# Optimization experiments

Measured on AMD Instinct MI355X. Metric: run time of the kernel, lower is better.

Reference implementation:

```python
import jax, jax.numpy as jnp
import numpy as np

N = 50000   # n_nodes
E = 800000  # n_edges (directed)
D = 64      # feature dim (in = hidden = out = 64 per source)


def setup_inputs() -> dict:
    key = jax.random.key(0)
    ks = jax.random.split(key, 16)
    s = 0.1  # init scale
    inp = {
        "x": jax.random.normal(ks[0], (N, D), jnp.float32),
        "edge_index": jax.random.randint(ks[1], (2, E), 0, N),
        # GCNConv 1
        "W1": jax.random.normal(ks[2], (D, 64), jnp.float32) * s,
        "b1": jnp.zeros((64,), jnp.float32),
        # TransformerConv (heads=1): query/key/value + root (skip) linear
        "Wq": jax.random.normal(ks[3], (64, 64), jnp.float32) * s,
        "bq": jnp.zeros((64,), jnp.float32),
        "Wk": jax.random.normal(ks[4], (64, 64), jnp.float32) * s,
        "bk": jnp.zeros((64,), jnp.float32),
        "Wv": jax.random.normal(ks[5], (64, 64), jnp.float32) * s,
        "bv": jnp.zeros((64,), jnp.float32),
        "Ws": jax.random.normal(ks[6], (64, 64), jnp.float32) * s,
        "bs": jnp.zeros((64,), jnp.float32),
        # GCNConv 2
        "W2": jax.random.normal(ks[7], (64, D), jnp.float32) * s,
        "b2": jnp.zeros((D,), jnp.float32),
    }
    return inp


def gcn_conv(x, W, b, src, dst, n):
    """PyG GCNConv: symmetric normalization with self-loops, then scatter-add."""
    xw = x @ W  # [N, F]
    loop = jnp.arange(n)
    src2 = jnp.concatenate([src, loop])
    dst2 = jnp.concatenate([dst, loop])
    deg = jax.ops.segment_sum(jnp.ones(src2.shape[0], xw.dtype), dst2, num_segments=n)
    dinv = jnp.where(deg > 0, jax.lax.rsqrt(deg), 0.0)
    norm = dinv[src2] * dinv[dst2]  # [E+N]
    out = jax.ops.segment_sum(xw[src2] * norm[:, None], dst2, num_segments=n)
    return out + b


def segment_softmax(logits, seg, n):
    m = jax.ops.segment_max(logits, seg, num_segments=n)
    e = jnp.exp(logits - m[seg])
    z = jax.ops.segment_sum(e, seg, num_segments=n)
    return e / z[seg]


def transformer_conv(x, Wq, bq, Wk, bk, Wv, bv, Ws, bs, src, dst, n):
    """PyG TransformerConv (heads=1, concat=True, root_weight=True)."""
    q = x @ Wq + bq  # [N, 64]
    k = x @ Wk + bk
    v = x @ Wv + bv
    scale = jax.lax.rsqrt(jnp.asarray(q.shape[-1], q.dtype))
    logits = jnp.sum(q[dst] * k[src], axis=-1) * scale  # [E]
    alpha = segment_softmax(logits, dst, n)
    aggr = jax.ops.segment_sum(v[src] * alpha[:, None], dst, num_segments=n)
    return aggr + x @ Ws + bs  # root/skip connection


def reference(x, edge_index, W1, b1, Wq, bq, Wk, bk, Wv, bv, Ws, bs, W2, b2):
    src, dst = edge_index[0], edge_index[1]
    n = x.shape[0]
    x1 = jax.nn.relu(gcn_conv(x, W1, b1, src, dst, n))
    x2 = transformer_conv(x1, Wq, bq, Wk, bk, Wv, bv, Ws, bs, src, dst, n)
    x3 = gcn_conv(x2, W2, b2, src, dst, n)
    return x3
```

## Files before the change

### kernel.cpp

```cpp
#include <hip/hip_runtime.h>
#include <math.h>


#define D 64
#define BKT_SHIFT 9
#define CAP 12288
#define CHUNK 4096

__device__ __forceinline__ unsigned short f2bf(float f) {
    unsigned int u = __float_as_uint(f);
    u += 0x7FFFu + ((u >> 16) & 1u);
    return (unsigned short)(u >> 16);
}
#define BF_LO(u) __uint_as_float((u) << 16)
#define BF_HI(u) __uint_as_float((u) & 0xFFFF0000u)


__global__ void init_gcursor(int* __restrict__ gcursor) {
    if (threadIdx.x < 128) gcursor[threadIdx.x] = 0;
}

__global__ __launch_bounds__(256) void binA_kernel(const int* __restrict__ src,
                                                   const int* __restrict__ dst,
                                                   int* __restrict__ gcursor,
                                                   unsigned int* __restrict__ staging,
                                                   int e, int nbkt) {
    __shared__ int cntB[128];
    __shared__ int offB[128];
    __shared__ int curB[128];
    __shared__ int gbase[128];
    __shared__ unsigned int pairs[CHUNK];
    __shared__ unsigned char bkt[CHUNK];

    int t = threadIdx.x;
    int e0 = blockIdx.x * CHUNK;
    int ecnt = min(CHUNK, e - e0);

    if (t < 128) cntB[t] = 0;
    __syncthreads();

    int myS[CHUNK / 256], myD[CHUNK / 256];
    #pragma unroll
    for (int i = 0; i < CHUNK / 256; ++i) {
        int idx = t + 256 * i;
        if (idx < ecnt) {
            myS[i] = src[e0 + idx];
            myD[i] = dst[e0 + idx];
            atomicAdd(&cntB[myD[i] >> BKT_SHIFT], 1);
        }
    }
    __syncthreads();
    if (t < 128) offB[t] = cntB[t];
    __syncthreads();
    for (int off = 1; off < 128; off <<= 1) {
        int add = (t < 128 && t >= off) ? offB[t - off] : 0;
        __syncthreads();
        if (t < 128) offB[t] += add;
        __syncthreads();
    }
    if (t < 128) {
        int excl = offB[t] - cntB[t];
        offB[t] = excl;
        curB[t] = excl;
        if (t < nbkt && cntB[t] > 0) gbase[t] = atomicAdd(&gcursor[t], cntB[t]);
    }
    __syncthreads();
    #pragma unroll
    for (int i = 0; i < CHUNK / 256; ++i) {
        int idx = t + 256 * i;
        if (idx < ecnt) {
            int b = myD[i] >> BKT_SHIFT;
            int p = atomicAdd(&curB[b], 1);
            pairs[p] = ((unsigned int)myD[i] << 16) | (unsigned int)myS[i];
            bkt[p] = (unsigned char)b;
        }
    }
    __syncthreads();
    for (int p = t; p < ecnt; p += 256) {
        int b = bkt[p];
        staging[(size_t)b * CAP + gbase[b] + (p - offB[b])] = pairs[p];
    }
}

__global__ __launch_bounds__(256) void binB_kernel(const int* __restrict__ gcursor,
                                                   const unsigned int* __restrict__ staging,
                                                   unsigned short* __restrict__ esrc,
                                                   int* __restrict__ cnt,
                                                   int* __restrict__ rowptr,
                                                   float* __restrict__ dinv,
                                                   int n, int nbkt) {
    __shared__ int bpre[128];
    __shared__ int c512[512];
    __shared__ int o512[512];
    int t = threadIdx.x;
    int b = blockIdx.x;

    if (t < 128) bpre[t] = (t < nbkt) ? gcursor[t] : 0;
    __syncthreads();
    for (int off = 1; off < 128; off <<= 1) {
        int add = (t < 128 && t >= off) ? bpre[t - off] : 0;
        __syncthreads();
        if (t < 128) bpre[t] += add;
        __syncthreads();
    }
    int base_b = (b == 0) ? 0 : bpre[b - 1];
    int cnt_b = gcursor[b];
    int lo = b << BKT_SHIFT;

    c512[t] = 0; c512[t + 256] = 0;
    __syncthreads();
    const unsigned int* st = staging + (size_t)b * CAP;
    for (int i = t; i < cnt_b; i += 256)
        atomicAdd(&c512[(int)(st[i] >> 16) - lo], 1);
    __syncthreads();
    o512[t] = c512[t]; o512[t + 256] = c512[t + 256];
    __syncthreads();
    for (int off = 1; off < 512; off <<= 1) {
        int a1 = (t >= off) ? o512[t - off] : 0;
        int a2 = o512[t + 256 - off];
        __syncthreads();
        o512[t] += a1; o512[t + 256] += a2;
        __syncthreads();
    }
    int e1 = o512[t] - c512[t];
    int e2 = o512[t + 256] - c512[t + 256];
    __syncthreads();
    o512[t] = e1; o512[t + 256] = e2;
    __syncthreads();
    for (int i = t; i < 512; i += 256) {
        int g = lo + i;
        if (g < n) {
            int c = c512[i];
            cnt[g] = c;
            rowptr[g] = base_b + o512[i];
            dinv[g] = rsqrtf((float)c + 1.0f);
        }
    }
    __syncthreads();
    for (int i = t; i < cnt_b; i += 256) {
        unsigned int pk = st[i];
        int local = (int)(pk >> 16) - lo;
        int p = atomicAdd(&o512[local], 1);
        esrc[base_b + p] = (unsigned short)(pk & 0xFFFFu);
    }
}

__global__ __launch_bounds__(256) void gemm64_bf16s(const float* __restrict__ X,
                                                    const float* __restrict__ W,
                                                    const float* __restrict__ dinv,
                                                    unsigned short* __restrict__ xs, int n) {
    __shared__ float sX[64][68];
    __shared__ float sW[64 * 64];
    int t = threadIdx.x;
    int base = blockIdx.x * 64;
    #pragma unroll
    for (int i = 0; i < 4; ++i) {
        int f = t * 4 + i * 1024;
        *(float4*)&sW[f] = *(const float4*)&W[f];
        int r = f >> 6, c = f & 63;
        int row = base + r;
        float4 xv = (row < n) ? *(const float4*)&X[(size_t)row * D + c]
                              : make_float4(0.f, 0.f, 0.f, 0.f);
        *(float4*)&sX[r][c] = xv;
    }
    __syncthreads();

    int cg = t & 15, rg = t >> 4;
    int j0 = cg * 4, r0 = rg * 4;
    float acc[4][4];
    #pragma unroll
    for (int a = 0; a < 4; ++a)
        #pragma unroll
        for (int c = 0; c < 4; ++c) acc[a][c] = 0.0f;

    #pragma unroll 4
    for (int kk = 0; kk < 64; kk += 4) {
        float4 w0 = *(const float4*)&sW[(kk + 0) * 64 + j0];
        float4 w1 = *(const float4*)&sW[(kk + 1) * 64 + j0];
        float4 w2 = *(const float4*)&sW[(kk + 2) * 64 + j0];
        float4 w3 = *(const float4*)&sW[(kk + 3) * 64 + j0];
        #pragma unroll
        for (int a = 0; a < 4; ++a) {
            float4 xv = *(const float4*)&sX[r0 + a][kk];
            acc[a][0] = fmaf(xv.x, w0.x, acc[a][0]); acc[a][1] = fmaf(xv.x, w0.y, acc[a][1]);
            acc[a][2] = fmaf(xv.x, w0.z, acc[a][2]); acc[a][3] = fmaf(xv.x, w0.w, acc[a][3]);
            acc[a][0] = fmaf(xv.y, w1.x, acc[a][0]); acc[a][1] = fmaf(xv.y, w1.y, acc[a][1]);
            acc[a][2] = fmaf(xv.y, w1.z, acc[a][2]); acc[a][3] = fmaf(xv.y, w1.w, acc[a][3]);
            acc[a][0] = fmaf(xv.z, w2.x, acc[a][0]); acc[a][1] = fmaf(xv.z, w2.y, acc[a][1]);
            acc[a][2] = fmaf(xv.z, w2.z, acc[a][2]); acc[a][3] = fmaf(xv.z, w2.w, acc[a][3]);
            acc[a][0] = fmaf(xv.w, w3.x, acc[a][0]); acc[a][1] = fmaf(xv.w, w3.y, acc[a][1]);
            acc[a][2] = fmaf(xv.w, w3.z, acc[a][2]); acc[a][3] = fmaf(xv.w, w3.w, acc[a][3]);
        }
    }

    #pragma unroll
    for (int a = 0; a < 4; ++a) {
        int row = base + r0 + a;
        if (row < n) {
            float dv = dinv[row];
            ushort4 h;
            h.x = f2bf(acc[a][0] * dv);
            h.y = f2bf(acc[a][1] * dv);
            h.z = f2bf(acc[a][2] * dv);
            h.w = f2bf(acc[a][3] * dv);
            *(ushort4*)&xs[(size_t)row * D + j0] = h;
        }
    }
}

__global__ __launch_bounds__(512) void fusedA_kernel(const unsigned short* __restrict__ xs,
                                                     const float* __restrict__ dinv,
                                                     const int* __restrict__ rowptr,
                                                     const int* __restrict__ cnt,
                                                     const unsigned short* __restrict__ esrc,
                                                     const float* __restrict__ b1,
                                                     const float* __restrict__ Wq,
                                                     const float* __restrict__ bq,
                                                     const float* __restrict__ Wk,
                                                     const float* __restrict__ bk,
                                                     const float* __restrict__ Wv,
                                                     const float* __restrict__ bv,
                                                     const float* __restrict__ Ws,
                                                     const float* __restrict__ bs,
                                                     float* __restrict__ Yq,
                                                     unsigned short* __restrict__ kv,
                                                     float* __restrict__ Ysk, int n) {
    __shared__ float sX[64][68];
    __shared__ unsigned short sWt[256 * 72];
    int t = threadIdx.x;
    int base = blockIdx.x * 64;
    int local = t >> 3, sub = t & 7;
    int j0 = sub * 8;
    int node = base + local;

    {
        int k0 = t >> 4;
        int c0 = (t & 15) * 4;
        #pragma unroll
        for (int m = 0; m < 4; ++m) {
            const float* W = (m == 0) ? Wq : (m == 1) ? Wk : (m == 2) ? Wv : Ws;
            #pragma unroll
            for (int h = 0; h < 2; ++h) {
                int k = k0 + 32 * h;
                float4 w = *(const float4*)&W[k * 64 + c0];
                sWt[(m * 64 + c0 + 0) * 72 + k] = f2bf(w.x);
                sWt[(m * 64 + c0 + 1) * 72 + k] = f2bf(w.y);
                sWt[(m * 64 + c0 + 2) * 72 + k] = f2bf(w.z);
                sWt[(m * 64 + c0 + 3) * 72 + k] = f2bf(w.w);
            }
        }
    }

    {
        float a[8] = {0.f, 0.f, 0.f, 0.f, 0.f, 0.f, 0.f, 0.f};
        float4 o0 = make_float4(0.f, 0.f, 0.f, 0.f);
        float4 o1 = make_float4(0.f, 0.f, 0.f, 0.f);
        if (node < n) {
            float dd = dinv[node];
            int start = rowptr[node], deg = cnt[node];
            uint4 sr = *(const uint4*)&xs[(size_t)node * D + j0];
            a[0] += BF_LO(sr.x); a[1] += BF_HI(sr.x);
            a[2] += BF_LO(sr.y); a[3] += BF_HI(sr.y);
            a[4] += BF_LO(sr.z); a[5] += BF_HI(sr.z);
            a[6] += BF_LO(sr.w); a[7] += BF_HI(sr.w);
            int i = 0;
            for (; i + 8 <= deg; i += 8) {
                uint4 r[8];
                #pragma unroll
                for (int u = 0; u < 8; ++u) {
                    int s = esrc[start + i + u];
                    r[u] = *(const uint4*)&xs[(size_t)s * D + j0];
                }
                #pragma unroll
                for (int u = 0; u < 8; ++u) {
                    a[0] += BF_LO(r[u].x); a[1] += BF_HI(r[u].x);
                    a[2] += BF_LO(r[u].y); a[3] += BF_HI(r[u].y);
                    a[4] += BF_LO(r[u].z); a[5] += BF_HI(r[u].z);
                    a[6] += BF_LO(r[u].w); a[7] += BF_HI(r[u].w);
                }
            }
            for (; i < deg; ++i) {
                int s = esrc[start + i];
                uint4 r = *(const uint4*)&xs[(size_t)s * D + j0];
                a[0] += BF_LO(r.x); a[1] += BF_HI(r.x);
                a[2] += BF_LO(r.y); a[3] += BF_HI(r.y);
                a[4] += BF_LO(r.z); a[5] += BF_HI(r.z);
                a[6] += BF_LO(r.w); a[7] += BF_HI(r.w);
            }
            float4 bb0 = *(const float4*)&b1[j0];
            float4 bb1 = *(const float4*)&b1[j0 + 4];
            o0.x = fmaxf(fmaf(dd, a[0], bb0.x), 0.f);
            o0.y = fmaxf(fmaf(dd, a[1], bb0.y), 0.f);
            o0.z = fmaxf(fmaf(dd, a[2], bb0.z), 0.f);
            o0.w = fmaxf(fmaf(dd, a[3], bb0.w), 0.f);
            o1.x = fmaxf(fmaf(dd, a[4], bb1.x), 0.f);
            o1.y = fmaxf(fmaf(dd, a[5], bb1.y), 0.f);
            o1.z = fmaxf(fmaf(dd, a[6], bb1.z), 0.f);
            o1.w = fmaxf(fmaf(dd, a[7], bb1.w), 0.f);
        }
        *(float4*)&sX[local][j0] = o0;
        *(float4*)&sX[local][j0 + 4] = o1;
    }
    __syncthreads();

    int rg = t >> 5;
    int cg = t & 31;
    float acc[4][8];
    #pragma unroll
    for (int a = 0; a < 4; ++a)
        #pragma unroll
        for (int j = 0; j < 8; ++j) acc[a][j] = 0.0f;

    #pragma unroll 2
    for (int s = 0; s < 8; ++s) {
        float xv[4][8];
        #pragma unroll
        for (int a = 0; a < 4; ++a) {
            int row = rg + 16 * a;
            float4 x0 = *(const float4*)&sX[row][s * 8];
            float4 x1 = *(const float4*)&sX[row][s * 8 + 4];
            xv[a][0] = x0.x; xv[a][1] = x0.y; xv[a][2] = x0.z; xv[a][3] = x0.w;
            xv[a][4] = x1.x; xv[a][5] = x1.y; xv[a][6] = x1.z; xv[a][7] = x1.w;
        }
        #pragma unroll
        for (int j = 0; j < 8; ++j) {
            uint4 wc = *(const uint4*)&sWt[(cg + 32 * j) * 72 + s * 8];
            float w0 = BF_LO(wc.x), w1 = BF_HI(wc.x);
            float w2 = BF_LO(wc.y), w3 = BF_HI(wc.y);
            float w4 = BF_LO(wc.z), w5 = BF_HI(wc.z);
            float w6 = BF_LO(wc.w), w7 = BF_HI(wc.w);
            #pragma unroll
            for (int a = 0; a < 4; ++a) {
                acc[a][j] = fmaf(xv[a][0], w0, acc[a][j]);
                acc[a][j] = fmaf(xv[a][1], w1, acc[a][j]);
                acc[a][j] = fmaf(xv[a][2], w2, acc[a][j]);
                acc[a][j] = fmaf(xv[a][3], w3, acc[a][j]);
                acc[a][j] = fmaf(xv[a][4], w4, acc[a][j]);
                acc[a][j] = fmaf(xv[a][5], w5, acc[a][j]);
                acc[a][j] = fmaf(xv[a][6], w6, acc[a][j]);
                acc[a][j] = fmaf(xv[a][7], w7, acc[a][j]);
            }
        }
    }

    float bq0 = bq[cg], bq1 = bq[cg + 32];
    float bk0 = bk[cg], bk1 = bk[cg + 32];
    float bv0 = bv[cg], bv1 = bv[cg + 32];
    float bs0 = bs[cg], bs1 = bs[cg + 32];
    #pragma unroll
    for (int a = 0; a < 4; ++a) {
        int row = base + rg + 16 * a;
        if (row < n) {
            Yq[(size_t)row * 64 + cg]        = (acc[a][0] + bq0) * 0.125f;
            Yq[(size_t)row * 64 + cg + 32]   = (acc[a][1] + bq1) * 0.125f;
            kv[(size_t)row * 128 + cg]       = f2bf(acc[a][2] + bk0);
            kv[(size_t)row * 128 + cg + 32]  = f2bf(acc[a][3] + bk1);
            kv[(size_t)row * 128 + 64 + cg]      = f2bf(acc[a][4] + bv0);
            kv[(size_t)row * 128 + 64 + cg + 32] = f2bf(acc[a][5] + bv1);
            Ysk[(size_t)row * 64 + cg]       = acc[a][6] + bs0;
            Ysk[(size_t)row * 64 + cg + 32]  = acc[a][7] + bs1;
        }
    }
}

__global__ __launch_bounds__(512) void fusedB_kernel(const float* __restrict__ q,
                                                     const unsigned short* __restrict__ kv,
                                                     const float* __restrict__ skip,
                                                     const float* __restrict__ dinv,
                                                     const int* __restrict__ rowptr,
                                                     const int* __restrict__ cnt,
                                                     const unsigned short* __restrict__ esrc,
                                                     const float* __restrict__ W2,
                                                     unsigned short* __restrict__ xs2, int n) {
    __shared__ float sX[64][68];
    __shared__ unsigned short sWt[64 * 72];
    int t = threadIdx.x;
    int base = blockIdx.x * 64;
    int local = t >> 3, sub = t & 7;
    int j0 = sub * 8;
    int node = base + local;

    {
        int k0 = t >> 4;
        int c0 = (t & 15) * 4;
        #pragma unroll
        for (int h = 0; h < 2; ++h) {
            int k = k0 + 32 * h;
            float4 w = *(const float4*)&W2[k * 64 + c0];
            sWt[(c0 + 0) * 72 + k] = f2bf(w.x);
            sWt[(c0 + 1) * 72 + k] = f2bf(w.y);
            sWt[(c0 + 2) * 72 + k] = f2bf(w.z);
            sWt[(c0 + 3) * 72 + k] = f2bf(w.w);
        }
    }

    {
        float4 o0 = make_float4(0.f, 0.f, 0.f, 0.f);
        float4 o1 = make_float4(0.f, 0.f, 0.f, 0.f);
        if (node < n) {
            int start = rowptr[node], deg = cnt[node];
            float4 q0 = *(const float4*)&q[(size_t)node * D + j0];
            float4 q1 = *(const float4*)&q[(size_t)node * D + j0 + 4];
            float4 s0 = *(const float4*)&skip[(size_t)node * D + j0];
            float4 s1 = *(const float4*)&skip[(size_t)node * D + j0 + 4];
            float z = 0.0f;
            float a[8] = {0.f, 0.f, 0.f, 0.f, 0.f, 0.f, 0.f, 0.f};
            int i = 0;
            for (; i + 8 <= deg; i += 8) {
                size_t ro[8];
                #pragma unroll
                for (int u = 0; u < 8; ++u)
                    ro[u] = (size_t)esrc[start + i + u] * 128;
                float w[8];
                {
                    uint4 kr[8];
                    #pragma unroll
                    for (int u = 0; u < 8; ++u)
                        kr[u] = *(const uint4*)&kv[ro[u] + j0];
                    float p[8];
                    #pragma unroll
                    for (int u = 0; u < 8; ++u)
                        p[u] = q0.x * BF_LO(kr[u].x) + q0.y * BF_HI(kr[u].x)
                             + q0.z * BF_LO(kr[u].y) + q0.w * BF_HI(kr[u].y)
                             + q1.x * BF_LO(kr[u].z) + q1.y * BF_HI(kr[u].z)
                             + q1.z * BF_LO(kr[u].w) + q1.w * BF_HI(kr[u].w);
                    #pragma unroll
                    for (int off = 1; off < 8; off <<= 1) {
                        #pragma unroll
                        for (int u = 0; u < 8; ++u) p[u] += __shfl_xor(p[u], off, 64);
                    }
                    #pragma unroll
                    for (int u = 0; u < 8; ++u) {
                        w[u] = __expf(p[u]);
                        z += w[u];
                    }
                }
                {
                    uint4 vr[8];
                    #pragma unroll
                    for (int u = 0; u < 8; ++u)
                        vr[u] = *(const uint4*)&kv[ro[u] + 64 + j0];
                    #pragma unroll
                    for (int u = 0; u < 8; ++u) {
                        a[0] = fmaf(w[u], BF_LO(vr[u].x), a[0]);
                        a[1] = fmaf(w[u], BF_HI(vr[u].x), a[1]);
                        a[2] = fmaf(w[u], BF_LO(vr[u].y), a[2]);
                        a[3] = fmaf(w[u], BF_HI(vr[u].y), a[3]);
                        a[4] = fmaf(w[u], BF_LO(vr[u].z), a[4]);
                        a[5] = fmaf(w[u], BF_HI(vr[u].z), a[5]);
                        a[6] = fmaf(w[u], BF_LO(vr[u].w), a[6]);
                        a[7] = fmaf(w[u], BF_HI(vr[u].w), a[7]);
                    }
                }
            }
            for (; i < deg; ++i) {
                size_t ro = (size_t)esrc[start + i] * 128;
                uint4 kr = *(const uint4*)&kv[ro + j0];
                uint4 vr = *(const uint4*)&kv[ro + 64 + j0];
                float p = q0.x * BF_LO(kr.x) + q0.y * BF_HI(kr.x)
                        + q0.z * BF_LO(kr.y) + q0.w * BF_HI(kr.y)
                        + q1.x * BF_LO(kr.z) + q1.y * BF_HI(kr.z)
                        + q1.z * BF_LO(kr.w) + q1.w * BF_HI(kr.w);
                #pragma unroll
                for (int off = 1; off < 8; off <<= 1) p += __shfl_xor(p, off, 64);
                float w = __expf(p);
                z += w;
                a[0] = fmaf(w, BF_LO(vr.x), a[0]); a[1] = fmaf(w, BF_HI(vr.x), a[1]);
                a[2] = fmaf(w, BF_LO(vr.y), a[2]); a[3] = fmaf(w, BF_HI(vr.y), a[3]);
                a[4] = fmaf(w, BF_LO(vr.z), a[4]); a[5] = fmaf(w, BF_HI(vr.z), a[5]);
                a[6] = fmaf(w, BF_LO(vr.w), a[6]); a[7] = fmaf(w, BF_HI(vr.w), a[7]);
            }
            if (deg > 0) {
                float inv = 1.0f / z;
                o0.x = fmaf(a[0], inv, s0.x); o0.y = fmaf(a[1], inv, s0.y);
                o0.z = fmaf(a[2], inv, s0.z); o0.w = fmaf(a[3], inv, s0.w);
                o1.x = fmaf(a[4], inv, s1.x); o1.y = fmaf(a[5], inv, s1.y);
                o1.z = fmaf(a[6], inv, s1.z); o1.w = fmaf(a[7], inv, s1.w);
            } else {
                o0 = s0; o1 = s1;
            }
        }
        *(float4*)&sX[local][j0] = o0;
        *(float4*)&sX[local][j0 + 4] = o1;
    }
    __syncthreads();

    int rg = t >> 4;
    int cg = t & 15;
    float acc[2][4];
    #pragma unroll
    for (int a = 0; a < 2; ++a)
        #pragma unroll
        for (int j = 0; j < 4; ++j) acc[a][j] = 0.0f;

    #pragma unroll 2
    for (int s = 0; s < 8; ++s) {
        float xv[2][8];
        #pragma unroll
        for (int a = 0; a < 2; ++a) {
            int row = rg + 32 * a;
            float4 x0 = *(const float4*)&sX[row][s * 8];
            float4 x1 = *(const float4*)&sX[row][s * 8 + 4];
            xv[a][0] = x0.x; xv[a][1] = x0.y; xv[a][2] = x0.z; xv[a][3] = x0.w;
            xv[a][4] = x1.x; xv[a][5] = x1.y; xv[a][6] = x1.z; xv[a][7] = x1.w;
        }
        #pragma unroll
        for (int j = 0; j < 4; ++j) {
            uint4 wc = *(const uint4*)&sWt[(cg + 16 * j) * 72 + s * 8];
            float w0 = BF_LO(wc.x), w1 = BF_HI(wc.x);
            float w2 = BF_LO(wc.y), w3 = BF_HI(wc.y);
            float w4 = BF_LO(wc.z), w5 = BF_HI(wc.z);
            float w6 = BF_LO(wc.w), w7 = BF_HI(wc.w);
            #pragma unroll
            for (int a = 0; a < 2; ++a) {
                acc[a][j] = fmaf(xv[a][0], w0, acc[a][j]);
                acc[a][j] = fmaf(xv[a][1], w1, acc[a][j]);
                acc[a][j] = fmaf(xv[a][2], w2, acc[a][j]);
                acc[a][j] = fmaf(xv[a][3], w3, acc[a][j]);
                acc[a][j] = fmaf(xv[a][4], w4, acc[a][j]);
                acc[a][j] = fmaf(xv[a][5], w5, acc[a][j]);
                acc[a][j] = fmaf(xv[a][6], w6, acc[a][j]);
                acc[a][j] = fmaf(xv[a][7], w7, acc[a][j]);
            }
        }
    }

    #pragma unroll
    for (int a = 0; a < 2; ++a) {
        int row = base + rg + 32 * a;
        if (row < n) {
            float dv = dinv[row];
            #pragma unroll
            for (int j = 0; j < 4; ++j)
                xs2[(size_t)row * 64 + cg + 16 * j] = f2bf(acc[a][j] * dv);
        }
    }
}

__global__ __launch_bounds__(256) void gcn_gather_kernel(const unsigned short* __restrict__ xs,
                                                         const float* __restrict__ dinv,
                                                         const int* __restrict__ rowptr,
                                                         const int* __restrict__ cnt,
                                                         const unsigned short* __restrict__ esrc,
                                                         const float* __restrict__ bias,
                                                         float* __restrict__ out,
                                                         int n, int relu) {
    int node = (blockIdx.x * blockDim.x + threadIdx.x) >> 6;
    if (node >= n) return;
    int lane = threadIdx.x & 63;
    int grp = lane >> 3;
    int sub = lane & 7;
    int j0 = sub * 8;

    int start = rowptr[node], deg = cnt[node];

    float a[8] = {0.f, 0.f, 0.f, 0.f, 0.f, 0.f, 0.f, 0.f};
    int i = grp;
    int sNext = (i < deg) ? esrc[start + i] : 0;
    for (; i < deg; i += 8) {
        int s = sNext;
        int in = i + 8;
        if (in < deg) sNext = esrc[start + in];
        uint4 r = *(const uint4*)&xs[(size_t)s * D + j0];
        a[0] += BF_LO(r.x); a[1] += BF_HI(r.x);
        a[2] += BF_LO(r.y); a[3] += BF_HI(r.y);
        a[4] += BF_LO(r.z); a[5] += BF_HI(r.z);
        a[6] += BF_LO(r.w); a[7] += BF_HI(r.w);
    }
    #pragma unroll
    for (int off = 8; off < 64; off <<= 1) {
        #pragma unroll
        for (int c = 0; c < 8; ++c) a[c] += __shfl_xor(a[c], off, 64);
    }

    if (grp == 0) {
        float dd = dinv[node];
        uint4 sr = *(const uint4*)&xs[(size_t)node * D + j0];
        a[0] += BF_LO(sr.x); a[1] += BF_HI(sr.x);
        a[2] += BF_LO(sr.y); a[3] += BF_HI(sr.y);
        a[4] += BF_LO(sr.z); a[5] += BF_HI(sr.z);
        a[6] += BF_LO(sr.w); a[7] += BF_HI(sr.w);
        float4 b0 = *(const float4*)&bias[j0];
        float4 b1 = *(const float4*)&bias[j0 + 4];
        float o[8];
        o[0] = fmaf(dd, a[0], b0.x); o[1] = fmaf(dd, a[1], b0.y);
        o[2] = fmaf(dd, a[2], b0.z); o[3] = fmaf(dd, a[3], b0.w);
        o[4] = fmaf(dd, a[4], b1.x); o[5] = fmaf(dd, a[5], b1.y);
        o[6] = fmaf(dd, a[6], b1.z); o[7] = fmaf(dd, a[7], b1.w);
        if (relu) {
            #pragma unroll
            for (int c = 0; c < 8; ++c) o[c] = fmaxf(o[c], 0.f);
        }
        *(float4*)&out[(size_t)node * D + j0] = make_float4(o[0], o[1], o[2], o[3]);
        *(float4*)&out[(size_t)node * D + j0 + 4] = make_float4(o[4], o[5], o[6], o[7]);
    }
}


extern "C" void kernel_launch(void* const* d_in, const int* in_sizes, int n_in,
                              void* d_out, int out_size, void* d_ws, size_t ws_size,
                              hipStream_t stream) {
    const float* x  = (const float*)d_in[0];
    const int*   ei = (const int*)d_in[1];
    const float* W1 = (const float*)d_in[2];
    const float* b1 = (const float*)d_in[3];
    const float* Wq = (const float*)d_in[4];
    const float* bq = (const float*)d_in[5];
    const float* Wk = (const float*)d_in[6];
    const float* bk = (const float*)d_in[7];
    const float* Wv = (const float*)d_in[8];
    const float* bv = (const float*)d_in[9];
    const float* Ws = (const float*)d_in[10];
    const float* bs = (const float*)d_in[11];
    const float* W2 = (const float*)d_in[12];
    const float* b2 = (const float*)d_in[13];
    float* out = (float*)d_out;

    const int n = in_sizes[0] / D;
    const int e = in_sizes[1] / 2;
    const int* src = ei;
    const int* dst = ei + e;
    const int n64 = n * D;
    const int nbkt = (n + (1 << BKT_SHIFT) - 1) >> BKT_SHIFT;

    char* w = (char*)d_ws;
    auto carve = [&](size_t bytes) {
        char* p = w;
        w += (bytes + 255) & ~(size_t)255;
        return p;
    };
    int* gcursor            = (int*)carve(128 * 4);
    unsigned int* staging   = (unsigned int*)carve((size_t)nbkt * CAP * 4);
    unsigned short* esrc    = (unsigned short*)carve((size_t)e * 2);
    int* cnt                = (int*)carve((size_t)n * 4);
    int* rowptr             = (int*)carve((size_t)n * 4);
    float* dinv             = (float*)carve((size_t)n * 4);
    float* bufQ             = (float*)carve((size_t)n64 * 4);
    unsigned short* xs      = (unsigned short*)carve((size_t)n64 * 2);
    unsigned short* kv      = (unsigned short*)carve((size_t)n64 * 4);

    const int nb_binA = (e + CHUNK - 1) / CHUNK;
    const int nb_nw   = (n + 3) / 4;
    const int nb_g    = (n + 63) / 64;

    init_gcursor<<<1, 128, 0, stream>>>(gcursor);
    binA_kernel<<<nb_binA, 256, 0, stream>>>(src, dst, gcursor, staging, e, nbkt);
    binB_kernel<<<nbkt, 256, 0, stream>>>(gcursor, staging, esrc, cnt, rowptr, dinv, n, nbkt);

    gemm64_bf16s<<<nb_g, 256, 0, stream>>>(x, W1, dinv, xs, n);

    fusedA_kernel<<<nb_g, 512, 0, stream>>>(xs, dinv, rowptr, cnt, esrc, b1,
                                            Wq, bq, Wk, bk, Wv, bv, Ws, bs,
                                            bufQ, kv, out, n);

    fusedB_kernel<<<nb_g, 512, 0, stream>>>(bufQ, kv, out, dinv,
                                            rowptr, cnt, esrc, W2, xs, n);

    gcn_gather_kernel<<<nb_nw, 256, 0, stream>>>(xs, dinv, rowptr, cnt, esrc,
                                                 b2, out, n, 0);
}
```

Before: 251.4 us.

## Use bf16 MFMA for dense projections in fused gather kernels

Replaces the scalar FMA mini-GEMMs in the two fused kernels (QKV/skip projection and the W2 projection) with MFMA 16x16x32 bf16 instructions. The activation tile in shared memory is now stored as packed bf16 instead of fp32, which halves its footprint. This removes a large block of VALU work, at the cost of rounding activations to bf16 before the matmul and a less coalesced store pattern from the MFMA output layout.

```diff
diff --git a/kernel.cpp b/kernel.cpp
--- a/kernel.cpp
+++ b/kernel.cpp
@@ -7,6 +7,9 @@
 #define CAP 12288
 #define CHUNK 4096
 
+typedef __attribute__((ext_vector_type(8))) short short8;
+typedef __attribute__((ext_vector_type(4))) float f32x4;
+
 __device__ __forceinline__ unsigned short f2bf(float f) {
     unsigned int u = __float_as_uint(f);
     u += 0x7FFFu + ((u >> 16) & 1u);
@@ -14,6 +17,10 @@
 }
 #define BF_LO(u) __uint_as_float((u) << 16)
 #define BF_HI(u) __uint_as_float((u) & 0xFFFF0000u)
+
+__device__ __forceinline__ unsigned int pack2(float a, float b) {
+    return (unsigned int)f2bf(a) | ((unsigned int)f2bf(b) << 16);
+}
 
 
 __global__ void init_gcursor(int* __restrict__ gcursor) {
@@ -225,7 +232,7 @@
                                                      float* __restrict__ Yq,
                                                      unsigned short* __restrict__ kv,
                                                      float* __restrict__ Ysk, int n) {
-    __shared__ float sX[64][68];
+    __shared__ unsigned short sXb[64][72];
     __shared__ unsigned short sWt[256 * 72];
     int t = threadIdx.x;
     int base = blockIdx.x * 64;
@@ -253,8 +260,7 @@
 
     {
         float a[8] = {0.f, 0.f, 0.f, 0.f, 0.f, 0.f, 0.f, 0.f};
-        float4 o0 = make_float4(0.f, 0.f, 0.f, 0.f);
-        float4 o1 = make_float4(0.f, 0.f, 0.f, 0.f);
+        uint4 pk = make_uint4(0u, 0u, 0u, 0u);
         if (node < n) {
             float dd = dinv[node];
             int start = rowptr[node], deg = cnt[node];
@@ -289,76 +295,72 @@
             }
             float4 bb0 = *(const float4*)&b1[j0];
             float4 bb1 = *(const float4*)&b1[j0 + 4];
-            o0.x = fmaxf(fmaf(dd, a[0], bb0.x), 0.f);
-            o0.y = fmaxf(fmaf(dd, a[1], bb0.y), 0.f);
-            o0.z = fmaxf(fmaf(dd, a[2], bb0.z), 0.f);
-            o0.w = fmaxf(fmaf(dd, a[3], bb0.w), 0.f);
-            o1.x = fmaxf(fmaf(dd, a[4], bb1.x), 0.f);
-            o1.y = fmaxf(fmaf(dd, a[5], bb1.y), 0.f);
-            o1.z = fmaxf(fmaf(dd, a[6], bb1.z), 0.f);
-            o1.w = fmaxf(fmaf(dd, a[7], bb1.w), 0.f);
-        }
-        *(float4*)&sX[local][j0] = o0;
-        *(float4*)&sX[local][j0 + 4] = o1;
-    }
-    __syncthreads();
-
-    int rg = t >> 5;
-    int cg = t & 31;
-    float acc[4][8];
-    #pragma unroll
-    for (int a = 0; a < 4; ++a)
-        #pragma unroll
-        for (int j = 0; j < 8; ++j) acc[a][j] = 0.0f;
-
-    #pragma unroll 2
-    for (int s = 0; s < 8; ++s) {
-        float xv[4][8];
-        #pragma unroll
-        for (int a = 0; a < 4; ++a) {
-            int row = rg + 16 * a;
-            float4 x0 = *(const float4*)&sX[row][s * 8];
-            float4 x1 = *(const float4*)&sX[row][s * 8 + 4];
-            xv[a][0] = x0.x; xv[a][1] = x0.y; xv[a][2] = x0.z; xv[a][3] = x0.w;
-            xv[a][4] = x1.x; xv[a][5] = x1.y; xv[a][6] = x1.z; xv[a][7] = x1.w;
-        }
-        #pragma unroll
-        for (int j = 0; j < 8; ++j) {
-            uint4 wc = *(const uint4*)&sWt[(cg + 32 * j) * 72 + s * 8];
-            float w0 = BF_LO(wc.x), w1 = BF_HI(wc.x);
-            float w2 = BF_LO(wc.y), w3 = BF_HI(wc.y);
-            float w4 = BF_LO(wc.z), w5 = BF_HI(wc.z);
-            float w6 = BF_LO(wc.w), w7 = BF_HI(wc.w);
+            float o0 = fmaxf(fmaf(dd, a[0], bb0.x), 0.f);
+            float o1 = fmaxf(fmaf(dd, a[1], bb0.y), 0.f);
+            float o2 = fmaxf(fmaf(dd, a[2], bb0.z), 0.f);
+            float o3 = fmaxf(fmaf(dd, a[3], bb0.w), 0.f);
+            float o4 = fmaxf(fmaf(dd, a[4], bb1.x), 0.f);
+            float o5 = fmaxf(fmaf(dd, a[5], bb1.y), 0.f);
+            float o6 = fmaxf(fmaf(dd, a[6], bb1.z), 0.f);
+            float o7 = fmaxf(fmaf(dd, a[7], bb1.w), 0.f);
+            pk.x = pack2(o0, o1); pk.y = pack2(o2, o3);
+            pk.z = pack2(o4, o5); pk.w = pack2(o6, o7);
+        }
+        *(uint4*)&sXb[local][j0] = pk;
+    }
+    __syncthreads();
+
+    int w = t >> 6;
+    int lane = t & 63;
+    int l15 = lane & 15;
+    int quad = lane >> 4;
+    int rt = w & 3;
+    int ct0 = (w >> 2) * 8;
+
+    short8 a0 = *(const short8*)&sXb[rt * 16 + l15][quad * 8];
+    short8 a1 = *(const short8*)&sXb[rt * 16 + l15][32 + quad * 8];
+
+    #pragma unroll
+    for (int tt = 0; tt < 8; ++tt) {
+        int ct = ct0 + tt;
+        int gcol = ct * 16 + l15;
+        const unsigned short* wcol = &sWt[(size_t)gcol * 72];
+        short8 bfr0 = *(const short8*)&wcol[quad * 8];
+        short8 bfr1 = *(const short8*)&wcol[32 + quad * 8];
+        f32x4 acc = {0.f, 0.f, 0.f, 0.f};
+        acc = __builtin_amdgcn_mfma_f32_16x16x32_bf16(a0, bfr0, acc, 0, 0, 0);
+        acc = __builtin_amdgcn_mfma_f32_16x16x32_bf16(a1, bfr1, acc, 0, 0, 0);
+
+        int m = gcol >> 6;
+        int col = gcol & 63;
+        if (m == 0) {
+            float bb = bq[col];
             #pragma unroll
-            for (int a = 0; a < 4; ++a) {
-                acc[a][j] = fmaf(xv[a][0], w0, acc[a][j]);
-                acc[a][j] = fmaf(xv[a][1], w1, acc[a][j]);
-                acc[a][j] = fmaf(xv[a][2], w2, acc[a][j]);
-                acc[a][j] = fmaf(xv[a][3], w3, acc[a][j]);
-                acc[a][j] = fmaf(xv[a][4], w4, acc[a][j]);
-                acc[a][j] = fmaf(xv[a][5], w5, acc[a][j]);
-                acc[a][j] = fmaf(xv[a][6], w6, acc[a][j]);
-                acc[a][j] = fmaf(xv[a][7], w7, acc[a][j]);
-            }
-        }
-    }
-
-    float bq0 = bq[cg], bq1 = bq[cg + 32];
-    float bk0 = bk[cg], bk1 = bk[cg + 32];
-    float bv0 = bv[cg], bv1 = bv[cg + 32];
-    float bs0 = bs[cg], bs1 = bs[cg + 32];
-    #pragma unroll
-    for (int a = 0; a < 4; ++a) {
-        int row = base + rg + 16 * a;
-        if (row < n) {
-            Yq[(size_t)row * 64 + cg]        = (acc[a][0] + bq0) * 0.125f;
-            Yq[(size_t)row * 64 + cg + 32]   = (acc[a][1] + bq1) * 0.125f;
-            kv[(size_t)row * 128 + cg]       = f2bf(acc[a][2] + bk0);
-            kv[(size_t)row * 128 + cg + 32]  = f2bf(acc[a][3] + bk1);
-            kv[(size_t)row * 128 + 64 + cg]      = f2bf(acc[a][4] + bv0);
-            kv[(size_t)row * 128 + 64 + cg + 32] = f2bf(acc[a][5] + bv1);
-            Ysk[(size_t)row * 64 + cg]       = acc[a][6] + bs0;
-            Ysk[(size_t)row * 64 + cg + 32]  = acc[a][7] + bs1;
+            for (int rgi = 0; rgi < 4; ++rgi) {
+                int row = base + rt * 16 + quad * 4 + rgi;
+                if (row < n) Yq[(size_t)row * 64 + col] = (acc[rgi] + bb) * 0.125f;
+            }
+        } else if (m == 1) {
+            float bb = bk[col];
+            #pragma unroll
+            for (int rgi = 0; rgi < 4; ++rgi) {
+                int row = base + rt * 16 + quad * 4 + rgi;
+                if (row < n) kv[(size_t)row * 128 + col] = f2bf(acc[rgi] + bb);
+            }
+        } else if (m == 2) {
+            float bb = bv[col];
+            #pragma unroll
+            for (int rgi = 0; rgi < 4; ++rgi) {
+                int row = base + rt * 16 + quad * 4 + rgi;
+                if (row < n) kv[(size_t)row * 128 + 64 + col] = f2bf(acc[rgi] + bb);
+            }
+        } else {
+            float bb = bs[col];
+            #pragma unroll
+            for (int rgi = 0; rgi < 4; ++rgi) {
+                int row = base + rt * 16 + quad * 4 + rgi;
+                if (row < n) Ysk[(size_t)row * 64 + col] = acc[rgi] + bb;
+            }
         }
     }
 }
@@ -372,7 +374,7 @@
                                                      const unsigned short* __restrict__ esrc,
                                                      const float* __restrict__ W2,
                                                      unsigned short* __restrict__ xs2, int n) {
-    __shared__ float sX[64][68];
+    __shared__ unsigned short sXb[64][72];
     __shared__ unsigned short sWt[64 * 72];
     int t = threadIdx.x;
     int base = blockIdx.x * 64;
@@ -395,8 +397,7 @@
     }
 
     {
-        float4 o0 = make_float4(0.f, 0.f, 0.f, 0.f);
-        float4 o1 = make_float4(0.f, 0.f, 0.f, 0.f);
+        uint4 pk = make_uint4(0u, 0u, 0u, 0u);
         if (node < n) {
             int start = rowptr[node], deg = cnt[node];
             float4 q0 = *(const float4*)&q[(size_t)node * D + j0];
@@ -411,7 +412,7 @@
                 #pragma unroll
                 for (int u = 0; u < 8; ++u)
                     ro[u] = (size_t)esrc[start + i + u] * 128;
-                float w[8];
+                float wgt[8];
                 {
                     uint4 kr[8];
                     #pragma unroll
@@ -431,8 +432,8 @@
                     }
                     #pragma unroll
                     for (int u = 0; u < 8; ++u) {
-                        w[u] = __expf(p[u]);
-                        z += w[u];
+                        wgt[u] = __expf(p[u]);
+                        z += wgt[u];
                     }
                 }
                 {
@@ -442,14 +443,14 @@
                         vr[u] = *(const uint4*)&kv[ro[u] + 64 + j0];
                     #pragma unroll
                     for (int u = 0; u < 8; ++u) {
-                        a[0] = fmaf(w[u], BF_LO(vr[u].x), a[0]);
-                        a[1] = fmaf(w[u], BF_HI(vr[u].x), a[1]);
-                        a[2] = fmaf(w[u], BF_LO(vr[u].y), a[2]);
-                        a[3] = fmaf(w[u], BF_HI(vr[u].y), a[3]);
-                        a[4] = fmaf(w[u], BF_LO(vr[u].z), a[4]);
-                        a[5] = fmaf(w[u], BF_HI(vr[u].z), a[5]);
-                        a[6] = fmaf(w[u], BF_LO(vr[u].w), a[6]);
-                        a[7] = fmaf(w[u], BF_HI(vr[u].w), a[7]);
+                        a[0] = fmaf(wgt[u], BF_LO(vr[u].x), a[0]);
+                        a[1] = fmaf(wgt[u], BF_HI(vr[u].x), a[1]);
+                        a[2] = fmaf(wgt[u], BF_LO(vr[u].y), a[2]);
+                        a[3] = fmaf(wgt[u], BF_HI(vr[u].y), a[3]);
+                        a[4] = fmaf(wgt[u], BF_LO(vr[u].z), a[4]);
+                        a[5] = fmaf(wgt[u], BF_HI(vr[u].z), a[5]);
+                        a[6] = fmaf(wgt[u], BF_LO(vr[u].w), a[6]);
+                        a[7] = fmaf(wgt[u], BF_HI(vr[u].w), a[7]);
                     }
                 }
             }
@@ -463,76 +464,58 @@
                         + q1.z * BF_LO(kr.w) + q1.w * BF_HI(kr.w);
                 #pragma unroll
                 for (int off = 1; off < 8; off <<= 1) p += __shfl_xor(p, off, 64);
-                float w = __expf(p);
-                z += w;
-                a[0] = fmaf(w, BF_LO(vr.x), a[0]); a[1] = fmaf(w, BF_HI(vr.x), a[1]);
-                a[2] = fmaf(w, BF_LO(vr.y), a[2]); a[3] = fmaf(w, BF_HI(vr.y), a[3]);
-                a[4] = fmaf(w, BF_LO(vr.z), a[4]); a[5] = fmaf(w, BF_HI(vr.z), a[5]);
-                a[6] = fmaf(w, BF_LO(vr.w), a[6]); a[7] = fmaf(w, BF_HI(vr.w), a[7]);
-            }
+                float wgt = __expf(p);
+                z += wgt;
+                a[0] = fmaf(wgt, BF_LO(vr.x), a[0]); a[1] = fmaf(wgt, BF_HI(vr.x), a[1]);
+                a[2] = fmaf(wgt, BF_LO(vr.y), a[2]); a[3] = fmaf(wgt, BF_HI(vr.y), a[3]);
+                a[4] = fmaf(wgt, BF_LO(vr.z), a[4]); a[5] = fmaf(wgt, BF_HI(vr.z), a[5]);
+                a[6] = fmaf(wgt, BF_LO(vr.w), a[6]); a[7] = fmaf(wgt, BF_HI(vr.w), a[7]);
+            }
+            float o[8];
             if (deg > 0) {
                 float inv = 1.0f / z;
-                o0.x = fmaf(a[0], inv, s0.x); o0.y = fmaf(a[1], inv, s0.y);
-                o0.z = fmaf(a[2], inv, s0.z); o0.w = fmaf(a[3], inv, s0.w);
-                o1.x = fmaf(a[4], inv, s1.x); o1.y = fmaf(a[5], inv, s1.y);
-                o1.z = fmaf(a[6], inv, s1.z); o1.w = fmaf(a[7], inv, s1.w);
+                o[0] = fmaf(a[0], inv, s0.x); o[1] = fmaf(a[1], inv, s0.y);
+                o[2] = fmaf(a[2], inv, s0.z); o[3] = fmaf(a[3], inv, s0.w);
+                o[4] = fmaf(a[4], inv, s1.x); o[5] = fmaf(a[5], inv, s1.y);
+                o[6] = fmaf(a[6], inv, s1.z); o[7] = fmaf(a[7], inv, s1.w);
             } else {
-                o0 = s0; o1 = s1;
-            }
-        }
-        *(float4*)&sX[local][j0] = o0;
-        *(float4*)&sX[local][j0 + 4] = o1;
-    }
-    __syncthreads();
-
-    int rg = t >> 4;
-    int cg = t & 15;
-    float acc[2][4];
-    #pragma unroll
-    for (int a = 0; a < 2; ++a)
+                o[0] = s0.x; o[1] = s0.y; o[2] = s0.z; o[3] = s0.w;
+                o[4] = s1.x; o[5] = s1.y; o[6] = s1.z; o[7] = s1.w;
+            }
+            pk.x = pack2(o[0], o[1]); pk.y = pack2(o[2], o[3]);
+            pk.z = pack2(o[4], o[5]); pk.w = pack2(o[6], o[7]);
+        }
+        *(uint4*)&sXb[local][j0] = pk;
+    }
+    __syncthreads();
+
+    int w = t >> 6;
+    int lane = t & 63;
+    int l15 = lane & 15;
+    int quad = lane >> 4;
+    int rt = w >> 1;
+    int ct0 = (w & 1) * 2;
+
+    short8 a0 = *(const short8*)&sXb[rt * 16 + l15][quad * 8];
+    short8 a1 = *(const short8*)&sXb[rt * 16 + l15][32 + quad * 8];
+
+    #pragma unroll
+    for (int tt = 0; tt < 2; ++tt) {
+        int ct = ct0 + tt;
+        int col = ct * 16 + l15;
+        const unsigned short* wcol = &sWt[(size_t)col * 72];
+        short8 bfr0 = *(const short8*)&wcol[quad * 8];
+        short8 bfr1 = *(const short8*)&wcol[32 + quad * 8];
+        f32x4 acc = {0.f, 0.f, 0.f, 0.f};
+        acc = __builtin_amdgcn_mfma_f32_16x16x32_bf16(a0, bfr0, acc, 0, 0, 0);
+        acc = __builtin_amdgcn_mfma_f32_16x16x32_bf16(a1, bfr1, acc, 0, 0, 0);
         #pragma unroll
-        for (int j = 0; j < 4; ++j) acc[a][j] = 0.0f;
-
-    #pragma unroll 2
-    for (int s = 0; s < 8; ++s) {
-        float xv[2][8];
-        #pragma unroll
-        for (int a = 0; a < 2; ++a) {
-            int row = rg + 32 * a;
-            float4 x0 = *(const float4*)&sX[row][s * 8];
-            float4 x1 = *(const float4*)&sX[row][s * 8 + 4];
-            xv[a][0] = x0.x; xv[a][1] = x0.y; xv[a][2] = x0.z; xv[a][3] = x0.w;
-            xv[a][4] = x1.x; xv[a][5] = x1.y; xv[a][6] = x1.z; xv[a][7] = x1.w;
-        }
-        #pragma unroll
-        for (int j = 0; j < 4; ++j) {
-            uint4 wc = *(const uint4*)&sWt[(cg + 16 * j) * 72 + s * 8];
-            float w0 = BF_LO(wc.x), w1 = BF_HI(wc.x);
-            float w2 = BF_LO(wc.y), w3 = BF_HI(wc.y);
-            float w4 = BF_LO(wc.z), w5 = BF_HI(wc.z);
-            float w6 = BF_LO(wc.w), w7 = BF_HI(wc.w);
-            #pragma unroll
-            for (int a = 0; a < 2; ++a) {
-                acc[a][j] = fmaf(xv[a][0], w0, acc[a][j]);
-                acc[a][j] = fmaf(xv[a][1], w1, acc[a][j]);
-                acc[a][j] = fmaf(xv[a][2], w2, acc[a][j]);
-                acc[a][j] = fmaf(xv[a][3], w3, acc[a][j]);
-                acc[a][j] = fmaf(xv[a][4], w4, acc[a][j]);
-                acc[a][j] = fmaf(xv[a][5], w5, acc[a][j]);
-                acc[a][j] = fmaf(xv[a][6], w6, acc[a][j]);
-                acc[a][j] = fmaf(xv[a][7], w7, acc[a][j]);
-            }
-        }
-    }
-
-    #pragma unroll
-    for (int a = 0; a < 2; ++a) {
-        int row = base + rg + 32 * a;
-        if (row < n) {
-            float dv = dinv[row];
-            #pragma unroll
-            for (int j = 0; j < 4; ++j)
-                xs2[(size_t)row * 64 + cg + 16 * j] = f2bf(acc[a][j] * dv);
+        for (int rgi = 0; rgi < 4; ++rgi) {
+            int row = base + rt * 16 + quad * 4 + rgi;
+            if (row < n) {
+                float dv = dinv[row];
+                xs2[(size_t)row * 64 + col] = f2bf(acc[rgi] * dv);
+            }
         }
     }
 }
```

Measured after the change: 235.5 us. 1.07x faster.
